# Kernel tuning notes

Measured on AMD Instinct MI355X. Metric: run time of the kernel, lower is better.

The kernel has to match this reference:

```python
import jax, jax.numpy as jnp
import numpy as np

N, V, C_IN, C_OUT = 8, 2048, 32, 64
ORDER, SUPPORT_LEN = 2, 3
BN_EPS = 1e-5


def _make_adj(key):
    a = jax.random.uniform(key, (N, V, V), dtype=jnp.float32)
    # row-normalize like a diffusion transition matrix
    return a / jnp.sum(a, axis=-1, keepdims=True)


def setup_inputs() -> dict:
    key = jax.random.key(0)
    ks = jax.random.split(key, 6)
    x = jax.random.normal(ks[0], (N, V, C_IN), dtype=jnp.float32)
    A0 = _make_adj(ks[1])
    A1 = _make_adj(ks[2])
    A2 = _make_adj(ks[3])
    c_in_total = (ORDER * SUPPORT_LEN + 1) * C_IN  # 224
    W = jax.random.normal(ks[4], (C_OUT, c_in_total), dtype=jnp.float32) / np.sqrt(c_in_total)
    b = jnp.zeros((C_OUT,), dtype=jnp.float32)
    gamma = jnp.ones((C_OUT,), dtype=jnp.float32)
    beta = jnp.zeros((C_OUT,), dtype=jnp.float32)
    return {"x": x, "A0": A0, "A1": A1, "A2": A2, "W": W, "b": b,
            "gamma": gamma, "beta": beta}


def reference(x, A0, A1, A2, W, b, gamma, beta):
    # nconv: einsum('nvl,nvw->nwl')
    nconv = lambda h, a: jnp.einsum('nvl,nvw->nwl', h, a)
    out = [x]
    for a in (A0, A1, A2):
        x1 = nconv(x, a)
        out.append(x1)
        for _ in range(2, ORDER + 1):
            x2 = nconv(x1, a)
            out.append(x2)
            x1 = x2
    h = jnp.concatenate(out, axis=-1)            # [N, V, 7*C_IN]
    # 1x1 Conv1d over channel axis == pointwise matmul + bias
    h = jnp.einsum('nvc,oc->nvo', h, W) + b      # [N, V, C_OUT]
    # BatchNorm1d (training-mode batch stats over batch and node dims)
    mean = jnp.mean(h, axis=(0, 1))
    var = jnp.var(h, axis=(0, 1))
    h = (h - mean) * jax.lax.rsqrt(var + BN_EPS) * gamma + beta
    # dropout p=0.0 -> identity
    return h
```

## Files before the change

kernel.cpp:

```cpp
#include <hip/hip_runtime.h>
#include <hip/hip_bf16.h>


#define V    2048
#define NB   8
#define CIN  32
#define COUT 64
#define CTOT 224

typedef __attribute__((ext_vector_type(8))) short bf16x8;
typedef __attribute__((ext_vector_type(16))) float f32x16;

static __device__ __forceinline__ short f2bf(float f) {
  __hip_bfloat16 h = __float2bfloat16(f);
  return *reinterpret_cast<short*>(&h);
}

__global__ __launch_bounds__(256) void nconv_mfma_kernel(
    const float* __restrict__ Adj, const float* __restrict__ Xin,
    float* __restrict__ Xout) {
  __shared__ float Lred[4][32][33];

  const int bid  = blockIdx.x;
  const int n    = bid >> 6;
  const int ws   = (bid & 63) * 32;
  const int t    = threadIdx.x;
  const int q    = t >> 6;
  const int lane = t & 63;
  const int g    = lane >> 5;
  const int mn   = lane & 31;

  const float* __restrict__ Ap =
      Adj + (size_t)n * V * V + (size_t)(q * 512 + 8 * g) * V + ws + mn;
  const float* __restrict__ Xp =
      Xin + (size_t)n * V * CIN + (q * 512 + 8 * g) * CIN + mn;

  float a0[8], a1[8], a2[8], a3[8];
  float x0[8], x1[8], x2[8], x3[8];

#define STAGE(S, C)                                                  \
  do {                                                               \
    const float* __restrict__ ap_ = Ap + (size_t)(C) * (16 * V);     \
    const float* __restrict__ xp_ = Xp + (C) * (16 * CIN);           \
    _Pragma("unroll") for (int j = 0; j < 8; ++j) {                  \
      a##S[j] = ap_[(size_t)j * V];                                  \
      x##S[j] = xp_[j * CIN];                                        \
    }                                                                \
  } while (0)

#define WAITV(N)                                         \
  do {                                                   \
    asm volatile("s_waitcnt vmcnt(" #N ")" ::: "memory");\
    __builtin_amdgcn_sched_barrier(0);                   \
  } while (0)

  f32x16 acc;
#pragma unroll
  for (int r = 0; r < 16; ++r) acc[r] = 0.f;

#define COMPUTE(S)                                                   \
  do {                                                               \
    bf16x8 aop_, bop_;                                               \
    _Pragma("unroll") for (int j = 0; j < 8; ++j) {                  \
      aop_[j] = f2bf(x##S[j]);             \
      bop_[j] = f2bf(a##S[j]);           \
    }                                                                \
    acc = __builtin_amdgcn_mfma_f32_32x32x16_bf16(aop_, bop_, acc,   \
                                                  0, 0, 0);          \
  } while (0)

  STAGE(0, 0);
  STAGE(1, 1);
  STAGE(2, 2);
#pragma unroll 1
  for (int it = 0; it < 7; ++it) {
    const int kb = it * 4;
    STAGE(3, kb + 3); WAITV(48); COMPUTE(0);
    STAGE(0, kb + 4); WAITV(48); COMPUTE(1);
    STAGE(1, kb + 5); WAITV(48); COMPUTE(2);
    STAGE(2, kb + 6); WAITV(48); COMPUTE(3);
  }
  STAGE(3, 31); WAITV(48); COMPUTE(0);
  WAITV(32); COMPUTE(1);
  WAITV(16); COMPUTE(2);
  WAITV(0);  COMPUTE(3);

#undef STAGE
#undef WAITV
#undef COMPUTE

#pragma unroll
  for (int r = 0; r < 16; ++r) {
    Lred[q][(r & 3) + 8 * (r >> 2) + 4 * g][mn] = acc[r];
  }
  __syncthreads();
  const int w  = t >> 3;
  const int l4 = t & 7;
  float4 o;
  float* op = &o.x;
#pragma unroll
  for (int i = 0; i < 4; ++i) {
    op[i] = Lred[0][l4 * 4 + i][w] + Lred[1][l4 * 4 + i][w] +
            Lred[2][l4 * 4 + i][w] + Lred[3][l4 * 4 + i][w];
  }
  *(float4*)(Xout + ((size_t)n * V + ws + w) * CIN + l4 * 4) = o;
}

__global__ __launch_bounds__(256) void conv_bn_stats_kernel(
    const float* __restrict__ W, const float* __restrict__ bias,
    const float* __restrict__ p0, const float* __restrict__ p1,
    const float* __restrict__ p2, const float* __restrict__ p3,
    const float* __restrict__ p4, const float* __restrict__ p5,
    const float* __restrict__ p6, float* __restrict__ hout,
    float* __restrict__ stats) {
  __shared__ float Wl[COUT * CTOT];
  __shared__ float Fl[64 * CTOT];
  const int t = threadIdx.x;
  const int R0 = blockIdx.x * 64;

#pragma unroll
  for (int s = 0; s < 14; ++s) {
    int fl = t + s * 256;
    int o = fl / 56, c4 = fl % 56;
    float4 wv = *(const float4*)(W + o * CTOT + c4 * 4);
    int c = c4 * 4;
    int csw = c ^ (((o >> 2) & 7) << 2);
    *(float4*)&Wl[o * CTOT + csw] = wv;
  }
  const float* parts[7] = {p0, p1, p2, p3, p4, p5, p6};
#pragma unroll
  for (int p = 0; p < 7; ++p) {
    const float* __restrict__ src = parts[p] + (size_t)R0 * CIN;
#pragma unroll
    for (int s = 0; s < 2; ++s) {
      int fl = t + s * 256;
      int r = fl >> 3, c4 = fl & 7;
      float4 v = *(const float4*)(src + r * CIN + c4 * 4);
      int c = p * 32 + c4 * 4;
      int csw = c ^ (((r >> 2) & 7) << 2);
      *(float4*)&Fl[r * CTOT + csw] = v;
    }
  }
  __syncthreads();

  const int rg = t & 15, og = t >> 4;
  const int r0 = rg * 4, o0 = og * 4;
  float acc[4][4];
#pragma unroll
  for (int i = 0; i < 4; ++i)
#pragma unroll
    for (int j = 0; j < 4; ++j) acc[i][j] = bias[o0 + j];

  const int fsw = (rg & 7) << 2;
  const int wsw = (og & 7) << 2;
  for (int cc = 0; cc < CTOT; cc += 4) {
    float4 f[4], w[4];
#pragma unroll
    for (int i = 0; i < 4; ++i)
      f[i] = *(const float4*)&Fl[(r0 + i) * CTOT + (cc ^ fsw)];
#pragma unroll
    for (int j = 0; j < 4; ++j)
      w[j] = *(const float4*)&Wl[(o0 + j) * CTOT + (cc ^ wsw)];
#pragma unroll
    for (int i = 0; i < 4; ++i)
#pragma unroll
      for (int j = 0; j < 4; ++j)
        acc[i][j] += f[i].x * w[j].x + f[i].y * w[j].y + f[i].z * w[j].z +
                     f[i].w * w[j].w;
  }

#pragma unroll
  for (int i = 0; i < 4; ++i) {
    *(float4*)(hout + (size_t)(R0 + r0 + i) * COUT + o0) =
        make_float4(acc[i][0], acc[i][1], acc[i][2], acc[i][3]);
  }

  __syncthreads();
  float* red = Fl;
#pragma unroll
  for (int j = 0; j < 4; ++j) {
    float s = acc[0][j] + acc[1][j] + acc[2][j] + acc[3][j];
    float qq = acc[0][j] * acc[0][j] + acc[1][j] * acc[1][j] +
               acc[2][j] * acc[2][j] + acc[3][j] * acc[3][j];
    red[(o0 + j) * 16 + rg] = s;
    red[1024 + (o0 + j) * 16 + rg] = qq;
  }
  __syncthreads();
  if (t < 128) {
    int o = t & 63, which = t >> 6;
    const float* b = red + which * 1024 + o * 16;
    float v = 0.f;
#pragma unroll
    for (int k = 0; k < 16; ++k) v += b[k];
    atomicAdd(stats + which * COUT + o, v);
  }
}

__global__ __launch_bounds__(256) void bn_apply_kernel(
    float* __restrict__ hout, const float* __restrict__ stats,
    const float* __restrict__ gamma, const float* __restrict__ beta) {
  const int i4 = blockIdx.x * 256 + threadIdx.x;
  const int oi = i4 & 15;
  float4 h = ((const float4*)hout)[i4];
  const float4 s = ((const float4*)stats)[oi];
  const float4 q = ((const float4*)(stats + COUT))[oi];
  const float4 g = ((const float4*)gamma)[oi];
  const float4 bb = ((const float4*)beta)[oi];
  const float inv = 1.f / 16384.f;
  float m, vv, rs;
  m = s.x * inv; vv = q.x * inv - m * m; rs = rsqrtf(vv + 1e-5f);
  h.x = (h.x - m) * rs * g.x + bb.x;
  m = s.y * inv; vv = q.y * inv - m * m; rs = rsqrtf(vv + 1e-5f);
  h.y = (h.y - m) * rs * g.y + bb.y;
  m = s.z * inv; vv = q.z * inv - m * m; rs = rsqrtf(vv + 1e-5f);
  h.z = (h.z - m) * rs * g.z + bb.z;
  m = s.w * inv; vv = q.w * inv - m * m; rs = rsqrtf(vv + 1e-5f);
  h.w = (h.w - m) * rs * g.w + bb.w;
  ((float4*)hout)[i4] = h;
}

extern "C" void kernel_launch(void* const* d_in, const int* in_sizes, int n_in,
                              void* d_out, int out_size, void* d_ws,
                              size_t ws_size, hipStream_t stream) {
  const float* x     = (const float*)d_in[0];
  const float* A0    = (const float*)d_in[1];
  const float* A1    = (const float*)d_in[2];
  const float* A2    = (const float*)d_in[3];
  const float* W     = (const float*)d_in[4];
  const float* b     = (const float*)d_in[5];
  const float* gamma = (const float*)d_in[6];
  const float* beta  = (const float*)d_in[7];
  float* out = (float*)d_out;

  char* ws = (char*)d_ws;
  float* stats = (float*)ws;
  const size_t BUF = (size_t)NB * V * CIN;
  float* x1_0 = (float*)(ws + 4096);
  float* x2_0 = x1_0 + BUF;
  float* x1_1 = x2_0 + BUF;
  float* x2_1 = x1_1 + BUF;
  float* x1_2 = x2_1 + BUF;
  float* x2_2 = x1_2 + BUF;

  hipMemsetAsync(stats, 0, 2 * COUT * sizeof(float), stream);

  dim3 g(512), blk(256);
  nconv_mfma_kernel<<<g, blk, 0, stream>>>(A0, x, x1_0);
  nconv_mfma_kernel<<<g, blk, 0, stream>>>(A0, x1_0, x2_0);
  nconv_mfma_kernel<<<g, blk, 0, stream>>>(A1, x, x1_1);
  nconv_mfma_kernel<<<g, blk, 0, stream>>>(A1, x1_1, x2_1);
  nconv_mfma_kernel<<<g, blk, 0, stream>>>(A2, x, x1_2);
  nconv_mfma_kernel<<<g, blk, 0, stream>>>(A2, x1_2, x2_2);

  conv_bn_stats_kernel<<<dim3(256), blk, 0, stream>>>(
      W, b, x, x1_0, x2_0, x1_1, x2_1, x1_2, x2_2, out, stats);
  bn_apply_kernel<<<dim3(1024), blk, 0, stream>>>(out, stats, gamma, beta);
}
```

Measured before the change: 211.4 us.

## Merge independent nconv launches into dual-job kernels to fill the GPU

Six sequential nconv launches are replaced by four, where the middle two each run two independent diffusion steps, the second hop of one adjacency and the first hop of the next, in a single grid. Block index parity selects which job each block computes. This raises the block count per launch and cuts launch and tail overhead. It also doubles the concurrent demand on HBM bandwidth for the adjacency reads.

```diff
diff --git a/kernel.cpp b/kernel.cpp
--- a/kernel.cpp
+++ b/kernel.cpp
@@ -16,14 +16,27 @@
   return *reinterpret_cast<short*>(&h);
 }
 
-__global__ __launch_bounds__(256) void nconv_mfma_kernel(
-    const float* __restrict__ Adj, const float* __restrict__ Xin,
-    float* __restrict__ Xout) {
+__global__ __launch_bounds__(256) void nconv_mfma_dual_kernel(
+    const float* __restrict__ AdjA, const float* __restrict__ XinA,
+    float* __restrict__ XoutA, const float* __restrict__ AdjB,
+    const float* __restrict__ XinB, float* __restrict__ XoutB) {
   __shared__ float Lred[4][32][33];
 
   const int bid  = blockIdx.x;
-  const int n    = bid >> 6;
-  const int ws   = (bid & 63) * 32;
+  int job, sub;
+  if (gridDim.x > 512) {
+    job = bid & 1;
+    sub = bid >> 1;
+  } else {
+    job = 0;
+    sub = bid;
+  }
+  const float* Adj  = job ? AdjB : AdjA;
+  const float* Xin  = job ? XinB : XinA;
+  float*       Xout = job ? XoutB : XoutA;
+
+  const int n    = sub >> 6;
+  const int ws   = (sub & 63) * 32;
   const int t    = threadIdx.x;
   const int q    = t >> 6;
   const int lane = t & 63;
@@ -244,13 +257,15 @@
 
   hipMemsetAsync(stats, 0, 2 * COUT * sizeof(float), stream);
 
-  dim3 g(512), blk(256);
-  nconv_mfma_kernel<<<g, blk, 0, stream>>>(A0, x, x1_0);
-  nconv_mfma_kernel<<<g, blk, 0, stream>>>(A0, x1_0, x2_0);
-  nconv_mfma_kernel<<<g, blk, 0, stream>>>(A1, x, x1_1);
-  nconv_mfma_kernel<<<g, blk, 0, stream>>>(A1, x1_1, x2_1);
-  nconv_mfma_kernel<<<g, blk, 0, stream>>>(A2, x, x1_2);
-  nconv_mfma_kernel<<<g, blk, 0, stream>>>(A2, x1_2, x2_2);
+  dim3 blk(256);
+  nconv_mfma_dual_kernel<<<dim3(512), blk, 0, stream>>>(
+      A0, x, x1_0, A0, x, x1_0);
+  nconv_mfma_dual_kernel<<<dim3(1024), blk, 0, stream>>>(
+      A0, x1_0, x2_0, A1, x, x1_1);
+  nconv_mfma_dual_kernel<<<dim3(1024), blk, 0, stream>>>(
+      A1, x1_1, x2_1, A2, x, x1_2);
+  nconv_mfma_dual_kernel<<<dim3(512), blk, 0, stream>>>(
+      A2, x1_2, x2_2, A2, x1_2, x2_2);
 
   conv_bn_stats_kernel<<<dim3(256), blk, 0, stream>>>(
       W, b, x, x1_0, x2_0, x1_1, x2_1, x1_2, x2_2, out, stats);
```

Result: no change. 210.1 us (-0.6%).
